# Performance work log

Measured on AMD Instinct MI355X. Metric: run time of the kernel, lower is better.

Reference implementation:

```python
import jax, jax.numpy as jnp
import numpy as np
import math


def setup_inputs() -> dict:
    rng = jax.random.key(0)
    k1, k2, k3 = jax.random.split(rng, 3)
    B, L, H, E = 2, 1024, 8, 64
    query = jax.random.normal(k1, (B, L, H, E), dtype=jnp.float32)
    key = jax.random.normal(k2, (B, L, H, E), dtype=jnp.float32)
    value = jax.random.normal(k3, (B, L, H, E), dtype=jnp.float32)
    mask_miss_k = jnp.zeros((B, L), dtype=bool)
    mask_miss_q = jnp.zeros((B, L), dtype=bool)
    pos = jnp.arange(B * L).reshape(B, L)
    causal_mask = 0  # unused by the module body
    # learned scalar parameters (nn.Parameter init values)
    log_gain_gate = jnp.float32(math.log(2.0))
    log_tau_gate = jnp.float32(math.log(0.5))
    log_gain_dir = jnp.float32(math.log(3.0))
    log_tau_dir = jnp.float32(math.log(0.3))
    return {
        "query": query, "key": key, "value": value,
        "mask_miss_k": mask_miss_k, "mask_miss_q": mask_miss_q,
        "pos": pos, "causal_mask": causal_mask,
        "log_gain_gate": log_gain_gate, "log_tau_gate": log_tau_gate,
        "log_gain_dir": log_gain_dir, "log_tau_dir": log_tau_dir,
    }


def reference(query, key, value, mask_miss_k, mask_miss_q, pos, causal_mask,
              log_gain_gate, log_tau_gate, log_gain_dir, log_tau_dir):
    # Multihead path: query (B,L,H,E). Eval mode, dropout p=0, dag_mask=None.
    B, L, H, E = query.shape
    scale = 1.0 / jnp.sqrt(jnp.float32(E))
    # scores: (B,H,L,S) with S == L
    scores = scale * jnp.einsum('blhe,bshe->bhls', query, key)
    scores_t = jnp.swapaxes(scores, -1, -2)
    S_sym = 0.5 * (scores + scores_t)       # symmetric part
    A_anti = 0.5 * (scores - scores_t)      # antisymmetric (Lie) part

    MAX_GAIN = 20.0
    gain_gate = jnp.clip(jnp.exp(log_gain_gate), 1e-3, MAX_GAIN)
    tau_gate = jnp.clip(jnp.exp(log_tau_gate), 1e-3, 10.0)
    gain_dir = jnp.clip(jnp.exp(log_gain_dir), 1e-3, MAX_GAIN)
    tau_dir = jnp.clip(jnp.exp(log_tau_dir), 1e-3, 10.0)

    gamma_att = gain_gate * jnp.tanh(S_sym / tau_gate)
    phi_att = gain_dir * jnp.tanh(A_anti / tau_dir)

    gate_probs = jax.nn.sigmoid(gamma_att)
    dir_probs = jax.nn.sigmoid(phi_att)
    dag_probs = gate_probs * dir_probs

    diag = jnp.eye(L, L, dtype=bool)  # P(i->i) = 0
    dag_probs = jnp.where(diag[None, None], 0.0, dag_probs)
    M = dag_probs  # eval branch; diagonal already zeroed (second fill is a no-op)

    att = jax.nn.relu(jnp.tanh(A_anti * gain_dir / tau_dir)) * M

    # entropy per query position (B,H,L)
    entropy = -jnp.sum(att * jnp.log(jnp.clip(att, 1e-8, None)), axis=-1)
    entropy = jnp.nan_to_num(entropy)

    # dropout p=0 -> identity; nan_to_num is a no-op on finite att
    V = jnp.einsum('bhls,bshd->blhd', att, value)  # (B,L,H,E)
    return V, att, entropy
```

## Files before the change

kernel.cpp:

```cpp
#include <hip/hip_runtime.h>
#include <math.h>

namespace {

typedef __bf16 bf16_t;
typedef bf16_t bf16x8 __attribute__((ext_vector_type(8)));
typedef bf16_t bf16x4 __attribute__((ext_vector_type(4)));
typedef bf16_t bf16x2 __attribute__((ext_vector_type(2)));
typedef float f32x4 __attribute__((ext_vector_type(4)));

constexpr int L = 1024;
constexpr int H = 8;
constexpr int E = 64;
constexpr int HE = H * E;
constexpr int BH = 16;
constexpr size_t PL = (size_t)BH * L * E;
constexpr float LOG2E = 1.4426950408889634f;
constexpr float LN2 = 0.6931471805599453f;

__device__ __forceinline__ float rcp_fast(float x) { return __builtin_amdgcn_rcpf(x); }
__device__ __forceinline__ float exp2_fast(float x) { return __builtin_amdgcn_exp2f(x); }
__device__ __forceinline__ float log2_fast(float x) { return __builtin_amdgcn_logf(x); }
__device__ __forceinline__ f32x4 mfma16(bf16x8 a, bf16x8 b, f32x4 c) {
  return __builtin_amdgcn_mfma_f32_16x16x32_bf16(a, b, c, 0, 0, 0);
}
__device__ __forceinline__ void split4(float4 x, bf16x4& hv, bf16x4& lv) {
  hv[0] = (bf16_t)x.x; lv[0] = (bf16_t)(x.x - (float)hv[0]);
  hv[1] = (bf16_t)x.y; lv[1] = (bf16_t)(x.y - (float)hv[1]);
  hv[2] = (bf16_t)x.z; lv[2] = (bf16_t)(x.z - (float)hv[2]);
  hv[3] = (bf16_t)x.w; lv[3] = (bf16_t)(x.w - (float)hv[3]);
}

__global__ __launch_bounds__(256) void k_prep(
    const float* __restrict__ q, const float* __restrict__ k,
    const float* __restrict__ v, bf16_t* __restrict__ ws,
    float* __restrict__ Vout, float* __restrict__ entr)
{
  const int bid = blockIdx.x;
  if (bid >= 256) {
    const int idx = (bid - 256) * 256 + threadIdx.x;
    const float4 z = make_float4(0.f, 0.f, 0.f, 0.f);
    if (idx < 262144) *(float4*)(Vout + (size_t)idx * 4) = z;
    else              *(float4*)(entr + (size_t)(idx - 262144) * 4) = z;
    return;
  }
  bf16_t* Qh = ws;
  bf16_t* Ql = ws + PL;
  bf16_t* Kh = ws + 2 * PL;
  bf16_t* Kl = ws + 3 * PL;
  bf16_t* VT = ws + 4 * PL;
  const int bh = bid >> 4, chunk = bid & 15;
  const int b = bh >> 3, h = bh & 7;
  const int tid = threadIdx.x, t8 = tid >> 4, c4 = tid & 15;
  __shared__ bf16_t Vb[64][72];

#pragma unroll
  for (int pass = 0; pass < 4; ++pass) {
    const int row = chunk * 64 + pass * 16 + t8;
    const size_t gin = ((size_t)(b * L + row) * H + h) * E + c4 * 4;
    const size_t gout = ((size_t)bh * L + row) * E + c4 * 4;
    float4 q4 = *(const float4*)(q + gin);
    float4 k4 = *(const float4*)(k + gin);
    float4 v4 = *(const float4*)(v + gin);
    bf16x4 hv, lv;
    split4(q4, hv, lv);
    *(bf16x4*)(Qh + gout) = hv; *(bf16x4*)(Ql + gout) = lv;
    split4(k4, hv, lv);
    *(bf16x4*)(Kh + gout) = hv; *(bf16x4*)(Kl + gout) = lv;
    const int sl = pass * 16 + t8;
    Vb[c4 * 4 + 0][sl] = (bf16_t)v4.x;
    Vb[c4 * 4 + 1][sl] = (bf16_t)v4.y;
    Vb[c4 * 4 + 2][sl] = (bf16_t)v4.z;
    Vb[c4 * 4 + 3][sl] = (bf16_t)v4.w;
  }
  __syncthreads();
#pragma unroll
  for (int pass = 0; pass < 2; ++pass) {
    const int idx = pass * 256 + tid;
    const int e = idx >> 3, ch = idx & 7;
    bf16x8 val = *(const bf16x8*)&Vb[e][ch * 8];
    *(bf16x8*)(VT + ((size_t)bh * E + e) * L + chunk * 64 + ch * 8) = val;
  }
}

__global__ __launch_bounds__(256, 3) void k_main(
    const bf16_t* __restrict__ ws,
    float* __restrict__ Vout, float* __restrict__ attg, float* __restrict__ entr,
    const float* __restrict__ p_lgg, const float* __restrict__ p_ltg,
    const float* __restrict__ p_lgd, const float* __restrict__ p_ltd)
{
  const bf16_t* Qh = ws;
  const bf16_t* Ql = ws + PL;
  const bf16_t* Kh = ws + 2 * PL;
  const bf16_t* Kl = ws + 3 * PL;
  const bf16_t* VT = ws + 4 * PL;

  __shared__ __align__(16) char smem[51200];
  bf16_t (*Kh_s)[72] = (bf16_t(*)[72])(smem);
  bf16_t (*Kl_s)[72] = (bf16_t(*)[72])(smem + 9216);
  bf16_t (*Qh_s)[72] = (bf16_t(*)[72])(smem + 18432);
  bf16_t (*Ql_s)[72] = (bf16_t(*)[72])(smem + 27648);
  bf16_t (*Vt_s)[72] = (bf16_t(*)[72])(smem + 36864);
  bf16_t (*attL)[40] = (bf16_t(*)[40])(smem + 46080);

  const int tid = threadIdx.x;
  const int w = tid >> 6, lane = tid & 63;
  const int c = lane & 15, qd = lane >> 4;
  const int lh = w & 1, sh = w >> 1;
  const int lt = blockIdx.x, bh = blockIdx.y, zb = blockIdx.z;
  const int b = bh >> 3, h = bh & 7;
  const int l0 = lt * 32;

  const float gg = fminf(fmaxf(__expf(p_lgg[0]), 1e-3f), 20.0f);
  const float tg = fminf(fmaxf(__expf(p_ltg[0]), 1e-3f), 10.0f);
  const float gd = fminf(fmaxf(__expf(p_lgd[0]), 1e-3f), 20.0f);
  const float td = fminf(fmaxf(__expf(p_ltd[0]), 1e-3f), 10.0f);
  const float A1 = 0.125f * (1.0f / tg) * LOG2E;
  const float A2 = 0.125f * (1.0f / td) * LOG2E;
  const float A3 = 0.125f * gd * (1.0f / td) * LOG2E;
  const float G1 = -gg * LOG2E, G1m2 = -2.0f * G1;
  const float G2 = -gd * LOG2E, G2m2 = -2.0f * G2;

  bf16x8 qaf[2][2], kaf[2][2];
  {
    const size_t aro = ((size_t)bh * L + l0 + lh * 16 + c) * E;
#pragma unroll
    for (int ks = 0; ks < 2; ++ks) {
      qaf[ks][0] = *(const bf16x8*)(Qh + aro + ks * 32 + qd * 8);
      qaf[ks][1] = *(const bf16x8*)(Ql + aro + ks * 32 + qd * 8);
      kaf[ks][0] = *(const bf16x8*)(Kh + aro + ks * 32 + qd * 8);
      kaf[ks][1] = *(const bf16x8*)(Kl + aro + ks * 32 + qd * 8);
    }
  }

  const int srow = tid >> 2, scol = (tid & 3) * 16;

  bf16x8 kh8a, kh8b, kl8a, kl8b, qh8a, qh8b, ql8a, ql8b, vt8a, vt8b;
  {
    const int s0 = zb * 4 * 64;
    const size_t off = ((size_t)bh * L + s0 + srow) * E + scol;
    kh8a = *(const bf16x8*)(Kh + off);   kh8b = *(const bf16x8*)(Kh + off + 8);
    kl8a = *(const bf16x8*)(Kl + off);   kl8b = *(const bf16x8*)(Kl + off + 8);
    qh8a = *(const bf16x8*)(Qh + off);   qh8b = *(const bf16x8*)(Qh + off + 8);
    ql8a = *(const bf16x8*)(Ql + off);   ql8b = *(const bf16x8*)(Ql + off + 8);
    const size_t voff = ((size_t)bh * E + srow) * L + s0 + scol;
    vt8a = *(const bf16x8*)(VT + voff);  vt8b = *(const bf16x8*)(VT + voff + 8);
  }

  f32x4 accv[4] = {};
  float ent[4] = {0.f, 0.f, 0.f, 0.f};

#pragma unroll
  for (int it = 0; it < 4; ++it) {
    const int s0 = (zb * 4 + it) * 64;
    const int s0n = ((zb * 4 + it + 1) & 15) * 64;

    __syncthreads();
    *(bf16x8*)&Kh_s[srow][scol]     = kh8a;
    *(bf16x8*)&Kh_s[srow][scol + 8] = kh8b;
    *(bf16x8*)&Kl_s[srow][scol]     = kl8a;
    *(bf16x8*)&Kl_s[srow][scol + 8] = kl8b;
    *(bf16x8*)&Qh_s[srow][scol]     = qh8a;
    *(bf16x8*)&Qh_s[srow][scol + 8] = qh8b;
    *(bf16x8*)&Ql_s[srow][scol]     = ql8a;
    *(bf16x8*)&Ql_s[srow][scol + 8] = ql8b;
    *(bf16x8*)&Vt_s[srow][scol]     = vt8a;
    *(bf16x8*)&Vt_s[srow][scol + 8] = vt8b;
    __syncthreads();

    {
      const size_t off = ((size_t)bh * L + s0n + srow) * E + scol;
      kh8a = *(const bf16x8*)(Kh + off);   kh8b = *(const bf16x8*)(Kh + off + 8);
      kl8a = *(const bf16x8*)(Kl + off);   kl8b = *(const bf16x8*)(Kl + off + 8);
      qh8a = *(const bf16x8*)(Qh + off);   qh8b = *(const bf16x8*)(Qh + off + 8);
      ql8a = *(const bf16x8*)(Ql + off);   ql8b = *(const bf16x8*)(Ql + off + 8);
      const size_t voff = ((size_t)bh * E + srow) * L + s0n + scol;
      vt8a = *(const bf16x8*)(VT + voff);  vt8b = *(const bf16x8*)(VT + voff + 8);
    }

    f32x4 acc1[2] = {}, acc2[2] = {};
#pragma unroll
    for (int nt = 0; nt < 2; ++nt) {
      const int brow = sh * 32 + nt * 16 + c;
#pragma unroll
      for (int ks = 0; ks < 2; ++ks) {
        bf16x8 kbh = *(const bf16x8*)&Kh_s[brow][ks * 32 + qd * 8];
        bf16x8 kbl = *(const bf16x8*)&Kl_s[brow][ks * 32 + qd * 8];
        bf16x8 qbh = *(const bf16x8*)&Qh_s[brow][ks * 32 + qd * 8];
        bf16x8 qbl = *(const bf16x8*)&Ql_s[brow][ks * 32 + qd * 8];
        acc1[nt] = mfma16(qaf[ks][0], kbh, acc1[nt]);
        acc1[nt] = mfma16(qaf[ks][0], kbl, acc1[nt]);
        acc1[nt] = mfma16(qaf[ks][1], kbh, acc1[nt]);
        acc2[nt] = mfma16(kaf[ks][0], qbh, acc2[nt]);
        acc2[nt] = mfma16(kaf[ks][1], qbh, acc2[nt]);
        acc2[nt] = mfma16(kaf[ks][0], qbl, acc2[nt]);
      }
    }

    float* arow = attg + ((size_t)bh * L + l0 + lh * 16 + qd * 4) * L + s0 + sh * 32;
#pragma unroll
    for (int nt = 0; nt < 2; ++nt) {
#pragma unroll
      for (int r = 0; r < 4; ++r) {
        float u = acc1[nt][r] + acc2[nt][r];
        float d = acc1[nt][r] - acc2[nt][r];
        float r1 = rcp_fast(exp2_fast(u * A1) + 1.f);
        float gate = rcp_fast(1.f + exp2_fast(fmaf(r1, G1m2, G1)));
        float r2 = rcp_fast(exp2_fast(d * A2) + 1.f);
        float dir  = rcp_fast(1.f + exp2_fast(fmaf(r2, G2m2, G2)));
        float t    = fmaf(rcp_fast(exp2_fast(d * A3) + 1.f), -2.f, 1.f);
        float a = fmaxf(t, 0.0f) * gate * dir;
        ent[r] -= a * log2_fast(fmaxf(a, 1e-8f));
        __builtin_nontemporal_store(a, arow + (size_t)r * L + nt * 16 + c);
        attL[w * 16 + qd * 4 + r][nt * 16 + c] = (bf16_t)a;
      }
    }
    asm volatile("s_waitcnt lgkmcnt(0)" ::: "memory");

    bf16x8 af = *(const bf16x8*)&attL[w * 16 + c][qd * 8];
#pragma unroll
    for (int ne = 0; ne < 4; ++ne) {
      bf16x8 bv = *(const bf16x8*)&Vt_s[ne * 16 + c][sh * 32 + qd * 8];
      accv[ne] = mfma16(af, bv, accv[ne]);
    }
  }

  __syncthreads();
  float (*red)[68] = (float(*)[68])smem;
  if (sh == 1) {
#pragma unroll
    for (int ne = 0; ne < 4; ++ne)
#pragma unroll
      for (int r = 0; r < 4; ++r)
        red[lh * 16 + qd * 4 + r][ne * 16 + c] = accv[ne][r];
  }
  __syncthreads();
  if (sh == 0) {
#pragma unroll
    for (int ne = 0; ne < 4; ++ne)
#pragma unroll
      for (int r = 0; r < 4; ++r) {
        float val = accv[ne][r] + red[lh * 16 + qd * 4 + r][ne * 16 + c];
        atomicAdd(Vout + ((size_t)(b * L + l0 + lh * 16 + qd * 4 + r) * H + h) * E +
                      ne * 16 + c,
                  val);
      }
  }
#pragma unroll
  for (int r = 0; r < 4; ++r) {
    float e = ent[r];
    e += __shfl_xor(e, 1);
    e += __shfl_xor(e, 2);
    e += __shfl_xor(e, 4);
    e += __shfl_xor(e, 8);
    if (c == 0)
      atomicAdd(entr + (size_t)bh * L + l0 + lh * 16 + qd * 4 + r, e * LN2);
  }
}

__device__ __forceinline__ float tanh_fast(float x) {
  return 1.0f - 2.0f * rcp_fast(__expf(2.0f * x) + 1.0f);
}
__device__ __forceinline__ float sigm_fast(float x) {
  return rcp_fast(1.0f + __expf(-x));
}
__device__ __forceinline__ void split_store(bf16_t* hi, bf16_t* lo, float4 x) {
  bf16x4 hv, lv;
  split4(x, hv, lv);
  *(bf16x4*)hi = hv;
  *(bf16x4*)lo = lv;
}

__global__ __launch_bounds__(128, 1) void fused_attn(
    const float* __restrict__ q, const float* __restrict__ kk,
    const float* __restrict__ v,
    float* __restrict__ Vout, float* __restrict__ attg, float* __restrict__ entr,
    const float* __restrict__ p_lgg, const float* __restrict__ p_ltg,
    const float* __restrict__ p_lgd, const float* __restrict__ p_ltd)
{
  constexpr int TM = 32;
  __shared__ bf16_t Qa_hi[TM][72], Qa_lo[TM][72];
  __shared__ bf16_t Ka_hi[TM][72], Ka_lo[TM][72];
  __shared__ bf16_t KQ_hi[64][72], KQ_lo[64][72];
  __shared__ bf16_t Vts[64][72];
  __shared__ float  T2ex[2][64][17];
  __shared__ bf16_t attLs[2][16][72];

  const int tid = threadIdx.x;
  const int w = tid >> 6;
  const int lane = tid & 63;
  const int c = lane & 15;
  const int qd = lane >> 4;
  const int t8 = tid >> 4;
  const int c4 = tid & 15;
  const int lt = blockIdx.x;
  const int bh = blockIdx.y;
  const int b = bh >> 3, h = bh & 7;
  const int l0 = lt * TM;

  const float gg = fminf(fmaxf(__expf(p_lgg[0]), 1e-3f), 20.0f);
  const float tg = fminf(fmaxf(__expf(p_ltg[0]), 1e-3f), 10.0f);
  const float gd = fminf(fmaxf(__expf(p_lgd[0]), 1e-3f), 20.0f);
  const float td = fminf(fmaxf(__expf(p_ltd[0]), 1e-3f), 10.0f);
  const float inv_tg = 1.0f / tg;
  const float inv_td = 1.0f / td;
  const float gd_inv_td = gd * inv_td;

  const float* qlbase = q  + ((size_t)(b * L + l0) * H + h) * E;
  const float* qsbase = q  + ((size_t)b * L * H + h) * E;
  const float* kbase  = kk + ((size_t)b * L * H + h) * E;
  const float* vbase  = v  + ((size_t)b * L * H + h) * E;

#pragma unroll
  for (int i = 0; i < 4; ++i) {
    int r = t8 + 8 * i;
    float4 qa = *(const float4*)(qlbase + (size_t)r * HE + c4 * 4);
    float4 ka = *(const float4*)(kbase + (size_t)(l0 + r) * HE + c4 * 4);
    split_store(&Qa_hi[r][c4 * 4], &Qa_lo[r][c4 * 4], qa);
    split_store(&Ka_hi[r][c4 * 4], &Ka_lo[r][c4 * 4], ka);
  }

  float4 kpre[8], qpre[8];
  float vpre[32];
#pragma unroll
  for (int i = 0; i < 8; ++i)
    kpre[i] = *(const float4*)(kbase + (size_t)(t8 + 8 * i) * HE + c4 * 4);
#pragma unroll
  for (int i = 0; i < 8; ++i)
    qpre[i] = *(const float4*)(qsbase + (size_t)(t8 + 8 * i) * HE + c4 * 4);
#pragma unroll
  for (int j = 0; j < 32; ++j)
    vpre[j] = vbase[(size_t)(w * 32 + j) * HE + lane];

  __syncthreads();

  bf16x8 qaf[2][2], kaf[2][2];
#pragma unroll
  for (int ks = 0; ks < 2; ++ks) {
    qaf[ks][0] = *(const bf16x8*)&Qa_hi[w * 16 + c][ks * 32 + qd * 8];
    qaf[ks][1] = *(const bf16x8*)&Qa_lo[w * 16 + c][ks * 32 + qd * 8];
    kaf[ks][0] = *(const bf16x8*)&Ka_hi[w * 16 + c][ks * 32 + qd * 8];
    kaf[ks][1] = *(const bf16x8*)&Ka_lo[w * 16 + c][ks * 32 + qd * 8];
  }

  f32x4 accv[4] = {};
  float ent[4] = {0.f, 0.f, 0.f, 0.f};
  const int gl_base = l0 + w * 16 + qd * 4;

  for (int it = 0; it < 16; ++it) {
    const int s0 = it * 64;
    const int snext = ((it + 1) & 15) * 64;

    __syncthreads();
#pragma unroll
    for (int i = 0; i < 8; ++i) {
      int r = t8 + 8 * i;
      split_store(&KQ_hi[r][c4 * 4], &KQ_lo[r][c4 * 4], kpre[i]);
    }
#pragma unroll
    for (int j = 0; j < 16; ++j) {
      bf16x2 p;
      p[0] = (bf16_t)vpre[2 * j];
      p[1] = (bf16_t)vpre[2 * j + 1];
      *(bf16x2*)&Vts[lane][w * 32 + 2 * j] = p;
    }
    __syncthreads();

#pragma unroll
    for (int i = 0; i < 8; ++i)
      kpre[i] = *(const float4*)(kbase + (size_t)(snext + t8 + 8 * i) * HE + c4 * 4);
#pragma unroll
    for (int j = 0; j < 32; ++j)
      vpre[j] = vbase[(size_t)(snext + w * 32 + j) * HE + lane];

    f32x4 acc1[4] = {};
#pragma unroll
    for (int nt = 0; nt < 4; ++nt) {
#pragma unroll
      for (int ks = 0; ks < 2; ++ks) {
        bf16x8 bhv = *(const bf16x8*)&KQ_hi[nt * 16 + c][ks * 32 + qd * 8];
        bf16x8 blv = *(const bf16x8*)&KQ_lo[nt * 16 + c][ks * 32 + qd * 8];
        acc1[nt] = mfma16(qaf[ks][0], bhv, acc1[nt]);
        acc1[nt] = mfma16(qaf[ks][0], blv, acc1[nt]);
        acc1[nt] = mfma16(qaf[ks][1], bhv, acc1[nt]);
      }
    }
    __syncthreads();

#pragma unroll
    for (int i = 0; i < 8; ++i) {
      int r = t8 + 8 * i;
      split_store(&KQ_hi[r][c4 * 4], &KQ_lo[r][c4 * 4], qpre[i]);
    }
    __syncthreads();

#pragma unroll
    for (int i = 0; i < 8; ++i)
      qpre[i] = *(const float4*)(qsbase + (size_t)(snext + t8 + 8 * i) * HE + c4 * 4);

    f32x4 acc2[4] = {};
#pragma unroll
    for (int mt = 0; mt < 4; ++mt) {
#pragma unroll
      for (int ks = 0; ks < 2; ++ks) {
        bf16x8 ahv = *(const bf16x8*)&KQ_hi[mt * 16 + c][ks * 32 + qd * 8];
        bf16x8 alv = *(const bf16x8*)&KQ_lo[mt * 16 + c][ks * 32 + qd * 8];
        acc2[mt] = mfma16(ahv, kaf[ks][0], acc2[mt]);
        acc2[mt] = mfma16(ahv, kaf[ks][1], acc2[mt]);
        acc2[mt] = mfma16(alv, kaf[ks][0], acc2[mt]);
      }
    }

#pragma unroll
    for (int mt = 0; mt < 4; ++mt)
#pragma unroll
      for (int r = 0; r < 4; ++r)
        T2ex[w][mt * 16 + qd * 4 + r][c] = acc2[mt][r];
    __syncthreads();

    float* attrow0 = attg + ((size_t)bh * L + gl_base) * L + s0;
#pragma unroll
    for (int nt = 0; nt < 4; ++nt) {
#pragma unroll
      for (int r = 0; r < 4; ++r) {
        float x = 0.125f * acc1[nt][r];
        float y = 0.125f * T2ex[w][nt * 16 + c][qd * 4 + r];
        float Ss = 0.5f * (x + y);
        float Aa = 0.5f * (x - y);
        float gate = sigm_fast(gg * tanh_fast(Ss * inv_tg));
        float dir  = sigm_fast(gd * tanh_fast(Aa * inv_td));
        float t    = tanh_fast(Aa * gd_inv_td);
        float a = fmaxf(t, 0.0f) * gate * dir;
        ent[r] -= a * __logf(fmaxf(a, 1e-8f));
        attrow0[(size_t)r * L + nt * 16 + c] = a;
        attLs[w][qd * 4 + r][nt * 16 + c] = (bf16_t)a;
      }
    }
    __syncthreads();

#pragma unroll
    for (int ks = 0; ks < 2; ++ks) {
      bf16x8 af = *(const bf16x8*)&attLs[w][c][ks * 32 + qd * 8];
#pragma unroll
      for (int ne = 0; ne < 4; ++ne) {
        bf16x8 bfv = *(const bf16x8*)&Vts[ne * 16 + c][ks * 32 + qd * 8];
        accv[ne] = mfma16(af, bfv, accv[ne]);
      }
    }
  }

#pragma unroll
  for (int r = 0; r < 4; ++r) {
    float* vb = Vout + ((size_t)(b * L + gl_base + r) * H + h) * E;
#pragma unroll
    for (int ne = 0; ne < 4; ++ne) vb[ne * 16 + c] = accv[ne][r];
    float e4 = ent[r];
    e4 += __shfl_xor(e4, 1);
    e4 += __shfl_xor(e4, 2);
    e4 += __shfl_xor(e4, 4);
    e4 += __shfl_xor(e4, 8);
    if (c == 0) entr[(size_t)bh * L + gl_base + r] = e4;
  }
}

}

extern "C" void kernel_launch(void* const* d_in, const int* in_sizes, int n_in,
                              void* d_out, int out_size, void* d_ws, size_t ws_size,
                              hipStream_t stream) {
  const float* q = (const float*)d_in[0];
  const float* k = (const float*)d_in[1];
  const float* v = (const float*)d_in[2];
  const float* p_lgg = (const float*)d_in[7];
  const float* p_ltg = (const float*)d_in[8];
  const float* p_lgd = (const float*)d_in[9];
  const float* p_ltd = (const float*)d_in[10];

  float* Vout = (float*)d_out;
  float* att  = Vout + 1048576;
  float* entr = att + 16777216;

  const size_t need = 5 * PL * sizeof(bf16_t);
  if (ws_size >= need) {
    bf16_t* ws = (bf16_t*)d_ws;
    k_prep<<<dim3(1296), 256, 0, stream>>>(q, k, v, ws, Vout, entr);
    k_main<<<dim3(32, 16, 4), 256, 0, stream>>>(
        ws, Vout, att, entr, p_lgg, p_ltg, p_lgd, p_ltd);
  } else {
    fused_attn<<<dim3(32, 16), 128, 0, stream>>>(
        q, k, v, Vout, att, entr, p_lgg, p_ltg, p_lgd, p_ltd);
  }
}
```

Baseline: 139.4 us.

## Exploit score antisymmetry: compute each tile pair once, split PV into separate kernel

The main kernel now processes unordered 64x64 tile pairs (I,J) and derives both att[I,J] and att[J,I] from one score computation. It relies on S_sym being symmetric and A_anti antisymmetric, so the transposed tile follows from the gate and negated direction terms, and it writes the transposed tile through shared memory. This roughly halves the QK^T MFMA and transcendental work. The PV product moves to a new kernel that rereads the fp32 attention matrix from global memory, which adds a 64 MB read and an extra launch in exchange for removing the Vout atomics and zero-fill.

```diff
diff --git a/kernel.cpp b/kernel.cpp
--- a/kernel.cpp
+++ b/kernel.cpp
@@ -34,14 +34,12 @@
 __global__ __launch_bounds__(256) void k_prep(
     const float* __restrict__ q, const float* __restrict__ k,
     const float* __restrict__ v, bf16_t* __restrict__ ws,
-    float* __restrict__ Vout, float* __restrict__ entr)
+    float* __restrict__ entr)
 {
   const int bid = blockIdx.x;
   if (bid >= 256) {
     const int idx = (bid - 256) * 256 + threadIdx.x;
-    const float4 z = make_float4(0.f, 0.f, 0.f, 0.f);
-    if (idx < 262144) *(float4*)(Vout + (size_t)idx * 4) = z;
-    else              *(float4*)(entr + (size_t)(idx - 262144) * 4) = z;
+    *(float4*)(entr + (size_t)idx * 4) = make_float4(0.f, 0.f, 0.f, 0.f);
     return;
   }
   bf16_t* Qh = ws;
@@ -83,9 +81,9 @@
   }
 }
 
-__global__ __launch_bounds__(256, 3) void k_main(
-    const bf16_t* __restrict__ ws,
-    float* __restrict__ Vout, float* __restrict__ attg, float* __restrict__ entr,
+__global__ __launch_bounds__(256, 4) void k_pair(
+    const bf16_t* __restrict__ ws, float* __restrict__ attg,
+    float* __restrict__ entr,
     const float* __restrict__ p_lgg, const float* __restrict__ p_ltg,
     const float* __restrict__ p_lgd, const float* __restrict__ p_ltd)
 {
@@ -93,23 +91,25 @@
   const bf16_t* Ql = ws + PL;
   const bf16_t* Kh = ws + 2 * PL;
   const bf16_t* Kl = ws + 3 * PL;
-  const bf16_t* VT = ws + 4 * PL;
-
-  __shared__ __align__(16) char smem[51200];
+
+  __shared__ __align__(16) char smem[36864];
   bf16_t (*Kh_s)[72] = (bf16_t(*)[72])(smem);
   bf16_t (*Kl_s)[72] = (bf16_t(*)[72])(smem + 9216);
   bf16_t (*Qh_s)[72] = (bf16_t(*)[72])(smem + 18432);
   bf16_t (*Ql_s)[72] = (bf16_t(*)[72])(smem + 27648);
-  bf16_t (*Vt_s)[72] = (bf16_t(*)[72])(smem + 36864);
-  bf16_t (*attL)[40] = (bf16_t(*)[40])(smem + 46080);
+  float  (*att2f)[68] = (float(*)[68])(smem);
 
   const int tid = threadIdx.x;
   const int w = tid >> 6, lane = tid & 63;
   const int c = lane & 15, qd = lane >> 4;
-  const int lh = w & 1, sh = w >> 1;
-  const int lt = blockIdx.x, bh = blockIdx.y, zb = blockIdx.z;
-  const int b = bh >> 3, h = bh & 7;
-  const int l0 = lt * 32;
+  const int bh = blockIdx.y;
+
+  const int pidx = blockIdx.x;
+  int I, J;
+  if (pidx < 112)      { const int kk = (pidx >> 4) + 1; I = pidx & 15; J = (I + kk) & 15; }
+  else if (pidx < 120) { I = pidx - 112; J = I + 8; }
+  else                 { I = pidx - 120; J = I; }
+  const bool diag = (I == J);
 
   const float gg = fminf(fmaxf(__expf(p_lgg[0]), 1e-3f), 20.0f);
   const float tg = fminf(fmaxf(__expf(p_ltg[0]), 1e-3f), 10.0f);
@@ -123,7 +123,7 @@
 
   bf16x8 qaf[2][2], kaf[2][2];
   {
-    const size_t aro = ((size_t)bh * L + l0 + lh * 16 + c) * E;
+    const size_t aro = ((size_t)bh * L + I * 64 + w * 16 + c) * E;
 #pragma unroll
     for (int ks = 0; ks < 2; ++ks) {
       qaf[ks][0] = *(const bf16x8*)(Qh + aro + ks * 32 + qd * 8);
@@ -132,130 +132,153 @@
       kaf[ks][1] = *(const bf16x8*)(Kl + aro + ks * 32 + qd * 8);
     }
   }
-
-  const int srow = tid >> 2, scol = (tid & 3) * 16;
-
-  bf16x8 kh8a, kh8b, kl8a, kl8b, qh8a, qh8b, ql8a, ql8b, vt8a, vt8b;
   {
-    const int s0 = zb * 4 * 64;
-    const size_t off = ((size_t)bh * L + s0 + srow) * E + scol;
-    kh8a = *(const bf16x8*)(Kh + off);   kh8b = *(const bf16x8*)(Kh + off + 8);
-    kl8a = *(const bf16x8*)(Kl + off);   kl8b = *(const bf16x8*)(Kl + off + 8);
-    qh8a = *(const bf16x8*)(Qh + off);   qh8b = *(const bf16x8*)(Qh + off + 8);
-    ql8a = *(const bf16x8*)(Ql + off);   ql8b = *(const bf16x8*)(Ql + off + 8);
-    const size_t voff = ((size_t)bh * E + srow) * L + s0 + scol;
-    vt8a = *(const bf16x8*)(VT + voff);  vt8b = *(const bf16x8*)(VT + voff + 8);
-  }
-
-  f32x4 accv[4] = {};
-  float ent[4] = {0.f, 0.f, 0.f, 0.f};
-
-#pragma unroll
-  for (int it = 0; it < 4; ++it) {
-    const int s0 = (zb * 4 + it) * 64;
-    const int s0n = ((zb * 4 + it + 1) & 15) * 64;
-
-    __syncthreads();
-    *(bf16x8*)&Kh_s[srow][scol]     = kh8a;
-    *(bf16x8*)&Kh_s[srow][scol + 8] = kh8b;
-    *(bf16x8*)&Kl_s[srow][scol]     = kl8a;
-    *(bf16x8*)&Kl_s[srow][scol + 8] = kl8b;
-    *(bf16x8*)&Qh_s[srow][scol]     = qh8a;
-    *(bf16x8*)&Qh_s[srow][scol + 8] = qh8b;
-    *(bf16x8*)&Ql_s[srow][scol]     = ql8a;
-    *(bf16x8*)&Ql_s[srow][scol + 8] = ql8b;
-    *(bf16x8*)&Vt_s[srow][scol]     = vt8a;
-    *(bf16x8*)&Vt_s[srow][scol + 8] = vt8b;
-    __syncthreads();
-
-    {
-      const size_t off = ((size_t)bh * L + s0n + srow) * E + scol;
-      kh8a = *(const bf16x8*)(Kh + off);   kh8b = *(const bf16x8*)(Kh + off + 8);
-      kl8a = *(const bf16x8*)(Kl + off);   kl8b = *(const bf16x8*)(Kl + off + 8);
-      qh8a = *(const bf16x8*)(Qh + off);   qh8b = *(const bf16x8*)(Qh + off + 8);
-      ql8a = *(const bf16x8*)(Ql + off);   ql8b = *(const bf16x8*)(Ql + off + 8);
-      const size_t voff = ((size_t)bh * E + srow) * L + s0n + scol;
-      vt8a = *(const bf16x8*)(VT + voff);  vt8b = *(const bf16x8*)(VT + voff + 8);
-    }
-
-    f32x4 acc1[2] = {}, acc2[2] = {};
-#pragma unroll
-    for (int nt = 0; nt < 2; ++nt) {
-      const int brow = sh * 32 + nt * 16 + c;
-#pragma unroll
-      for (int ks = 0; ks < 2; ++ks) {
-        bf16x8 kbh = *(const bf16x8*)&Kh_s[brow][ks * 32 + qd * 8];
-        bf16x8 kbl = *(const bf16x8*)&Kl_s[brow][ks * 32 + qd * 8];
-        bf16x8 qbh = *(const bf16x8*)&Qh_s[brow][ks * 32 + qd * 8];
-        bf16x8 qbl = *(const bf16x8*)&Ql_s[brow][ks * 32 + qd * 8];
-        acc1[nt] = mfma16(qaf[ks][0], kbh, acc1[nt]);
-        acc1[nt] = mfma16(qaf[ks][0], kbl, acc1[nt]);
-        acc1[nt] = mfma16(qaf[ks][1], kbh, acc1[nt]);
-        acc2[nt] = mfma16(kaf[ks][0], qbh, acc2[nt]);
-        acc2[nt] = mfma16(kaf[ks][1], qbh, acc2[nt]);
-        acc2[nt] = mfma16(kaf[ks][0], qbl, acc2[nt]);
+    const int srow = tid >> 2, scol = (tid & 3) * 16;
+    const size_t pj = ((size_t)bh * L + J * 64 + srow) * E + scol;
+    *(bf16x8*)&Kh_s[srow][scol]     = *(const bf16x8*)(Kh + pj);
+    *(bf16x8*)&Kh_s[srow][scol + 8] = *(const bf16x8*)(Kh + pj + 8);
+    *(bf16x8*)&Kl_s[srow][scol]     = *(const bf16x8*)(Kl + pj);
+    *(bf16x8*)&Kl_s[srow][scol + 8] = *(const bf16x8*)(Kl + pj + 8);
+    *(bf16x8*)&Qh_s[srow][scol]     = *(const bf16x8*)(Qh + pj);
+    *(bf16x8*)&Qh_s[srow][scol + 8] = *(const bf16x8*)(Qh + pj + 8);
+    *(bf16x8*)&Ql_s[srow][scol]     = *(const bf16x8*)(Ql + pj);
+    *(bf16x8*)&Ql_s[srow][scol + 8] = *(const bf16x8*)(Ql + pj + 8);
+  }
+  __syncthreads();
+
+  f32x4 acc1[4] = {}, acc2[4] = {};
+#pragma unroll
+  for (int nt = 0; nt < 4; ++nt) {
+    const int brow = nt * 16 + c;
+#pragma unroll
+    for (int ks = 0; ks < 2; ++ks) {
+      bf16x8 kbh = *(const bf16x8*)&Kh_s[brow][ks * 32 + qd * 8];
+      bf16x8 kbl = *(const bf16x8*)&Kl_s[brow][ks * 32 + qd * 8];
+      bf16x8 qbh = *(const bf16x8*)&Qh_s[brow][ks * 32 + qd * 8];
+      bf16x8 qbl = *(const bf16x8*)&Ql_s[brow][ks * 32 + qd * 8];
+      acc1[nt] = mfma16(qaf[ks][0], kbh, acc1[nt]);
+      acc1[nt] = mfma16(qaf[ks][0], kbl, acc1[nt]);
+      acc1[nt] = mfma16(qaf[ks][1], kbh, acc1[nt]);
+      acc2[nt] = mfma16(kaf[ks][0], qbh, acc2[nt]);
+      acc2[nt] = mfma16(kaf[ks][1], qbh, acc2[nt]);
+      acc2[nt] = mfma16(kaf[ks][0], qbl, acc2[nt]);
+    }
+  }
+  __syncthreads();
+
+  float entL[4] = {0.f, 0.f, 0.f, 0.f};
+  float entS[4] = {0.f, 0.f, 0.f, 0.f};
+  float* arow = attg + ((size_t)bh * L + I * 64 + w * 16 + qd * 4) * L + (size_t)J * 64;
+  if (!diag) {
+#pragma unroll
+    for (int nt = 0; nt < 4; ++nt) {
+      f32x4 a2v;
+#pragma unroll
+      for (int r = 0; r < 4; ++r) {
+        const float u = acc1[nt][r] + acc2[nt][r];
+        const float d = acc1[nt][r] - acc2[nt][r];
+        const float r1 = rcp_fast(exp2_fast(u * A1) + 1.f);
+        const float gate = rcp_fast(1.f + exp2_fast(fmaf(r1, G1m2, G1)));
+        const float r2 = rcp_fast(exp2_fast(d * A2) + 1.f);
+        const float dir = rcp_fast(1.f + exp2_fast(fmaf(r2, G2m2, G2)));
+        const float t = fmaf(rcp_fast(exp2_fast(d * A3) + 1.f), -2.f, 1.f);
+        const float gdp = gate * dir;
+        const float a1 = fmaxf(t, 0.f) * gdp;
+        const float a2 = fmaxf(-t, 0.f) * (gate - gdp);
+        const float la = log2_fast(fmaxf(a1 + a2, 1e-8f));
+        entL[r] -= a1 * la;
+        entS[nt] -= a2 * la;
+        __builtin_nontemporal_store(a1, arow + (size_t)r * L + nt * 16 + c);
+        a2v[r] = a2;
       }
-    }
-
-    float* arow = attg + ((size_t)bh * L + l0 + lh * 16 + qd * 4) * L + s0 + sh * 32;
-#pragma unroll
-    for (int nt = 0; nt < 2; ++nt) {
+      *(f32x4*)&att2f[nt * 16 + c][w * 16 + qd * 4] = a2v;
+    }
+  } else {
+#pragma unroll
+    for (int nt = 0; nt < 4; ++nt)
 #pragma unroll
       for (int r = 0; r < 4; ++r) {
-        float u = acc1[nt][r] + acc2[nt][r];
-        float d = acc1[nt][r] - acc2[nt][r];
-        float r1 = rcp_fast(exp2_fast(u * A1) + 1.f);
-        float gate = rcp_fast(1.f + exp2_fast(fmaf(r1, G1m2, G1)));
-        float r2 = rcp_fast(exp2_fast(d * A2) + 1.f);
-        float dir  = rcp_fast(1.f + exp2_fast(fmaf(r2, G2m2, G2)));
-        float t    = fmaf(rcp_fast(exp2_fast(d * A3) + 1.f), -2.f, 1.f);
-        float a = fmaxf(t, 0.0f) * gate * dir;
-        ent[r] -= a * log2_fast(fmaxf(a, 1e-8f));
-        __builtin_nontemporal_store(a, arow + (size_t)r * L + nt * 16 + c);
-        attL[w * 16 + qd * 4 + r][nt * 16 + c] = (bf16_t)a;
+        const float u = acc1[nt][r] + acc2[nt][r];
+        const float d = acc1[nt][r] - acc2[nt][r];
+        const float r1 = rcp_fast(exp2_fast(u * A1) + 1.f);
+        const float gate = rcp_fast(1.f + exp2_fast(fmaf(r1, G1m2, G1)));
+        const float r2 = rcp_fast(exp2_fast(d * A2) + 1.f);
+        const float dir = rcp_fast(1.f + exp2_fast(fmaf(r2, G2m2, G2)));
+        const float t = fmaf(rcp_fast(exp2_fast(d * A3) + 1.f), -2.f, 1.f);
+        const float a1 = fmaxf(t, 0.f) * gate * dir;
+        const float la = log2_fast(fmaxf(a1, 1e-8f));
+        entL[r] -= a1 * la;
+        __builtin_nontemporal_store(a1, arow + (size_t)r * L + nt * 16 + c);
       }
-    }
-    asm volatile("s_waitcnt lgkmcnt(0)" ::: "memory");
-
-    bf16x8 af = *(const bf16x8*)&attL[w * 16 + c][qd * 8];
-#pragma unroll
-    for (int ne = 0; ne < 4; ++ne) {
-      bf16x8 bv = *(const bf16x8*)&Vt_s[ne * 16 + c][sh * 32 + qd * 8];
-      accv[ne] = mfma16(af, bv, accv[ne]);
-    }
-  }
-
+  }
   __syncthreads();
-  float (*red)[68] = (float(*)[68])smem;
-  if (sh == 1) {
-#pragma unroll
-    for (int ne = 0; ne < 4; ++ne)
-#pragma unroll
-      for (int r = 0; r < 4; ++r)
-        red[lh * 16 + qd * 4 + r][ne * 16 + c] = accv[ne][r];
-  }
-  __syncthreads();
-  if (sh == 0) {
-#pragma unroll
-    for (int ne = 0; ne < 4; ++ne)
-#pragma unroll
-      for (int r = 0; r < 4; ++r) {
-        float val = accv[ne][r] + red[lh * 16 + qd * 4 + r][ne * 16 + c];
-        atomicAdd(Vout + ((size_t)(b * L + l0 + lh * 16 + qd * 4 + r) * H + h) * E +
-                      ne * 16 + c,
-                  val);
-      }
-  }
+
+  if (!diag) {
+    const int sr = tid >> 2, scb = (tid & 3) * 16;
+    float* orow = attg + ((size_t)bh * L + J * 64 + sr) * L + (size_t)I * 64 + scb;
+#pragma unroll
+    for (int j = 0; j < 4; ++j) {
+      f32x4 vv = *(const f32x4*)&att2f[sr][scb + j * 4];
+      __builtin_nontemporal_store(vv, (f32x4*)(orow + j * 4));
+    }
+  }
+
 #pragma unroll
   for (int r = 0; r < 4; ++r) {
-    float e = ent[r];
+    float e = entL[r];
     e += __shfl_xor(e, 1);
     e += __shfl_xor(e, 2);
     e += __shfl_xor(e, 4);
     e += __shfl_xor(e, 8);
     if (c == 0)
-      atomicAdd(entr + (size_t)bh * L + l0 + lh * 16 + qd * 4 + r, e * LN2);
-  }
+      atomicAdd(entr + (size_t)bh * L + I * 64 + w * 16 + qd * 4 + r, e * LN2);
+  }
+  if (!diag) {
+#pragma unroll
+    for (int nt = 0; nt < 4; ++nt) {
+      float e = entS[nt];
+      e += __shfl_xor(e, 16);
+      e += __shfl_xor(e, 32);
+      if (lane < 16)
+        atomicAdd(entr + (size_t)bh * L + J * 64 + nt * 16 + c, e * LN2);
+    }
+  }
+}
+
+__global__ __launch_bounds__(256, 4) void k_pv(
+    const bf16_t* __restrict__ ws, const float* __restrict__ attg,
+    float* __restrict__ Vout)
+{
+  const bf16_t* VT = ws + 4 * PL;
+  const int tid = threadIdx.x, w = tid >> 6, lane = tid & 63;
+  const int c = lane & 15, qd = lane >> 4;
+  const int lt = blockIdx.x;
+  const int bh = blockIdx.y;
+  const int b = bh >> 3, h = bh & 7;
+  const int l0 = lt * 16;
+
+  const float* abase = attg + ((size_t)bh * L + l0 + c) * L;
+  const bf16_t* vrow = VT + ((size_t)bh * E + w * 16 + c) * L;
+
+  f32x4 acc = {};
+  for (int st = 0; st < 16; ++st) {
+#pragma unroll
+    for (int ks = 0; ks < 2; ++ks) {
+      const int so = st * 64 + ks * 32 + qd * 8;
+      bf16x8 bv = *(const bf16x8*)(vrow + so);
+      f32x4 a0 = *(const f32x4*)(abase + so);
+      f32x4 a1v = *(const f32x4*)(abase + so + 4);
+      bf16x8 af;
+      af[0] = (bf16_t)a0[0];  af[1] = (bf16_t)a0[1];
+      af[2] = (bf16_t)a0[2];  af[3] = (bf16_t)a0[3];
+      af[4] = (bf16_t)a1v[0]; af[5] = (bf16_t)a1v[1];
+      af[6] = (bf16_t)a1v[2]; af[7] = (bf16_t)a1v[3];
+      acc = mfma16(af, bv, acc);
+    }
+  }
+#pragma unroll
+  for (int r = 0; r < 4; ++r)
+    Vout[((size_t)(b * L + l0 + qd * 4 + r) * H + h) * E + w * 16 + c] = acc[r];
 }
 
 __device__ __forceinline__ float tanh_fast(float x) {
@@ -483,9 +506,10 @@
   const size_t need = 5 * PL * sizeof(bf16_t);
   if (ws_size >= need) {
     bf16_t* ws = (bf16_t*)d_ws;
-    k_prep<<<dim3(1296), 256, 0, stream>>>(q, k, v, ws, Vout, entr);
-    k_main<<<dim3(32, 16, 4), 256, 0, stream>>>(
-        ws, Vout, att, entr, p_lgg, p_ltg, p_lgd, p_ltd);
+    k_prep<<<dim3(272), 256, 0, stream>>>(q, k, v, ws, entr);
+    k_pair<<<dim3(136, 16), 256, 0, stream>>>(
+        ws, att, entr, p_lgg, p_ltg, p_lgd, p_ltd);
+    k_pv<<<dim3(64, 16), 256, 0, stream>>>(ws, att, Vout);
   } else {
     fused_attn<<<dim3(32, 16), 128, 0, stream>>>(
         q, k, v, Vout, att, entr, p_lgg, p_ltg, p_lgd, p_ltd);
```

New measurement: 197.1 us. 41.4% more time.
